# Kernel optimization log

Measured on AMD Instinct MI355X. Metric: run time of the kernel, lower is better.

The kernel has to match this reference:

```python
import jax, jax.numpy as jnp
import numpy as np

B, T, F = 2048, 2048, 12   # n_locations, seq_len, input features
E, P, H = 4, 4, 4          # embedding_dim, pre_hidden, n_hidden
D1, D3, OUT = 4, 6, 1      # hidden dense sizes, output_dim


def setup_inputs() -> dict:
    key = jax.random.key(0)
    ks = jax.random.split(key, 14)
    s = lambda k, shape, fan_in: jax.random.normal(k, shape, jnp.float32) / np.sqrt(fan_in)
    return {
        "x": jax.random.normal(ks[0], (B, T, F), jnp.float32),
        "embed": s(ks[1], (B, E), 1.0),            # Embed table, rows = arange(n_locations)
        "W1": s(ks[2], (F + E, D1), F + E), "b1": jnp.zeros((D1,), jnp.float32),
        "W2": s(ks[3], (D1, P), D1),        "b2": jnp.zeros((P,), jnp.float32),
        "Wi": s(ks[4], (P, H), P),          "bi": jnp.zeros((H,), jnp.float32),
        "Wh": s(ks[5], (H, H), H),          # SimpleCell h2h has no bias in flax
        "W3": s(ks[6], (H, D3), H),         "b3": jnp.zeros((D3,), jnp.float32),
        "W4": s(ks[7], (D3, OUT), D3),      "b4": jnp.zeros((OUT,), jnp.float32),
    }


def reference(x, embed, W1, b1, W2, b2, Wi, bi, Wh, W3, b3, W4, b4):
    # loc = Embed(arange(n_locations)) -> the full table; broadcast over time.
    Tn = x.shape[1]
    loc = jnp.broadcast_to(embed[:, None, :], (embed.shape[0], Tn, embed.shape[1]))
    h = jnp.concatenate([x, loc], axis=-1)            # [B, T, F+E]
    h = jax.nn.relu(h @ W1 + b1)                      # Dense(4) + relu (dropout: no-op, deterministic)
    h = h @ W2 + b2                                   # Dense(pre_hidden)
    # SimpleCell: h_t = tanh(Dense_i(x_t) + Dense_h(h_{t-1})); precompute input proj.
    xi = h @ Wi + bi                                  # [B, T, H]
    h0 = jnp.zeros((x.shape[0], Wh.shape[0]), x.dtype)

    def step(carry, xt):
        new_h = jnp.tanh(xt + carry @ Wh)
        return new_h, new_h

    _, ys = jax.lax.scan(step, h0, jnp.swapaxes(xi, 0, 1))  # scan over time: [T, B, H]
    y = jnp.swapaxes(ys, 0, 1)                        # [B, T, H]
    y = jax.nn.relu(y @ W3 + b3)                      # Dense(6) + relu
    return y @ W4 + b4                                # Dense(output_dim)
```

## Files before the change

### kernel.cpp

```cpp
#include <hip/hip_runtime.h>
#include <hip/hip_fp16.h>


using u32 = unsigned int;
using u16 = unsigned short;

#define B_N 2048
#define T_N 2048

typedef __fp16 f16x2 __attribute__((ext_vector_type(2)));

__device__ __forceinline__ float bfh(u16 v){ return __uint_as_float(((u32)v) << 16); }
__device__ __forceinline__ float lo16(u32 u){ return __uint_as_float(u << 16); }
__device__ __forceinline__ float hi16(u32 u){ return __uint_as_float(u & 0xFFFF0000u); }
__device__ __forceinline__ u16 f2bf(float f){
  u32 u = __float_as_uint(f);
  return (u16)((u + 0x7FFFu + ((u >> 16) & 1u)) >> 16);
}
__device__ __forceinline__ float h2f(u16 h){ return __half2float(__ushort_as_half(h)); }
__device__ __forceinline__ u32 pk2(float a, float b){
  union { f16x2 h; u32 u; } cv;
  cv.h = __builtin_amdgcn_cvt_pkrtz(a, b);
  return cv.u;
}

__global__ void k_setup(const void* __restrict__ xraw,
                        const void* __restrict__ embed, const void* __restrict__ W1,
                        const void* __restrict__ b1, const void* __restrict__ W2,
                        const void* __restrict__ b2, const void* __restrict__ Wi,
                        const void* __restrict__ bi, const void* __restrict__ Wh,
                        const void* __restrict__ W3, const void* __restrict__ b3,
                        const void* __restrict__ W4, const void* __restrict__ b4,
                        float* __restrict__ cbuf)
{
  const float S = 2.8853900817779268f;
  const int tid = threadIdx.x;
  __shared__ float sflag;

  if (tid < 64) {
    const u16* xu = (const u16*)xraw;
    u32 e = (xu[2*tid] >> 7) & 0xFF;
    unsigned long long m = __ballot(e >= 110 && e <= 140);
    if (tid == 0) {
      float f = (__popcll(m) < 32) ? 1.0f : 0.0f;
      sflag = f;
      cbuf[126] = f;
    }
  }
  __syncthreads();
  const bool f32 = sflag > 0.5f;
  auto ld = [&](const void* p, int i) -> float {
    return f32 ? ((const float*)p)[i] : bfh(((const u16*)p)[i]);
  };

  if (tid < 48) {
    cbuf[tid] = ld(W1, tid);
  } else if (tid < 64) {
    int i = tid - 48, r = i >> 2, c = i & 3;
    float s = 0.f;
    for (int p = 0; p < 4; ++p) s += ld(W2, r*4+p) * ld(Wi, p*4+c);
    cbuf[48 + i] = S * s;
  } else if (tid < 68) {
    int c = tid - 64;
    float s = ld(bi, c);
    for (int p = 0; p < 4; ++p) s += ld(b2, p) * ld(Wi, p*4+c);
    float sw = 0.f;
    for (int k = 0; k < 4; ++k) sw += ld(Wh, k*4+c);
    cbuf[64 + c] = S * s + S * sw;
  } else if (tid < 84) {
    int i = tid - 68;
    cbuf[68 + i] = -2.f * S * ld(Wh, i);
  } else if (tid < 108) {
    cbuf[tid] = ld(W3, tid - 84);
  } else if (tid < 114) {
    cbuf[tid] = ld(b3, tid - 108);
  } else if (tid < 120) {
    cbuf[tid] = ld(W4, tid - 114);
  } else if (tid == 120) {
    cbuf[120] = ld(b4, 0);
  }
  for (int b = tid; b < B_N; b += blockDim.x) {
    for (int c = 0; c < 4; ++c) {
      float s = ld(b1, c);
      for (int e = 0; e < 4; ++e) s += ld(embed, b*4+e) * ld(W1, (12+e)*4+c);
      cbuf[128 + b*4 + c] = s;
    }
  }
}

__global__ __launch_bounds__(256) void k_xi(const void* __restrict__ xraw,
                                            const float* __restrict__ cbuf,
                                            float* __restrict__ xi2)
{
  __shared__ u32 sx[12320];
  const int tid = threadIdx.x;
  const int b0 = (blockIdx.x >> 4) << 3;
  const int t0 = (blockIdx.x & 15) << 7;
  const bool f32 = cbuf[126] > 0.5f;

  const int RS  = f32 ? 1540 : 772;
  const int CPT = f32 ? 12 : 6;
  const int K   = f32 ? 12 : 6;

  {
    const int r = tid >> 5, c = tid & 31;
    const size_t rowbase_u32 = ((size_t)(b0 + r) * T_N + t0) * (size_t)CPT;
    const uint4* gsrc = (const uint4*)((const u32*)xraw + rowbase_u32);
    uint4* ldst = (uint4*)(sx + r * RS);
    for (int k = 0; k < K; ++k)
      ldst[c + 32*k] = gsrc[c + 32*k];
  }
  __syncthreads();

  float W1f[48];
#pragma unroll
  for (int i = 0; i < 48; ++i) W1f[i] = cbuf[i];
  float Wc[16];
#pragma unroll
  for (int i = 0; i < 16; ++i) Wc[i] = cbuf[48+i];
  float bc[4];
#pragma unroll
  for (int i = 0; i < 4; ++i) bc[i] = cbuf[64+i];

  const int r = tid & 7, t4l = tid >> 3;
  const int b = b0 + r;
  const int T4 = (t0 >> 2) + t4l;
  float p1[4];
#pragma unroll
  for (int i = 0; i < 4; ++i) p1[i] = cbuf[128 + b*4 + i];

  float acc[4][4];
#pragma unroll
  for (int ti = 0; ti < 4; ++ti) {
    const u32* sp = sx + r * RS + (t4l*4 + ti) * CPT;
    float xf[12];
    if (f32) {
#pragma unroll
      for (int f = 0; f < 12; ++f) xf[f] = __uint_as_float(sp[f]);
    } else {
#pragma unroll
      for (int w = 0; w < 6; ++w) {
        u32 u = sp[w];
        xf[2*w]   = lo16(u);
        xf[2*w+1] = hi16(u);
      }
    }
    float h1[4];
#pragma unroll
    for (int c = 0; c < 4; ++c) {
      float s = p1[c];
#pragma unroll
      for (int f = 0; f < 12; ++f) s = fmaf(xf[f], W1f[f*4+c], s);
      h1[c] = fmaxf(s, 0.f);
    }
#pragma unroll
    for (int c = 0; c < 4; ++c) {
      float s = bc[c];
#pragma unroll
      for (int k = 0; k < 4; ++k) s = fmaf(h1[k], Wc[k*4+c], s);
      acc[c][ti] = s;
    }
  }
  float4* dst = (float4*)xi2 + ((size_t)T4 * B_N + b) * 4;
#pragma unroll
  for (int jj = 0; jj < 4; ++jj)
    dst[jj] = make_float4(acc[jj][0], acc[jj][1], acc[jj][2], acc[jj][3]);
}

template<int CTRL>
__device__ __forceinline__ float dppf(float v) {
  return __int_as_float(__builtin_amdgcn_mov_dpp(__float_as_int(v), CTRL, 0xF, 0xF, true));
}

__global__ __launch_bounds__(64) void k_scan(const float* __restrict__ cbuf,
                                             const float* __restrict__ xi2,
                                             u32* __restrict__ hbuf)
{
  const int g = blockIdx.x * 64 + threadIdx.x;
  const int b = g >> 2, j = g & 3;
  const float u0 = cbuf[68 + (j<<2) + j];
  const float u1 = cbuf[68 + ((j^1)<<2) + j];
  const float u2 = cbuf[68 + ((j^2)<<2) + j];
  const float u3 = cbuf[68 + ((j^3)<<2) + j];

  const float4* xp = (const float4*)xi2 + (size_t)b*4 + j;
  uint2* hp = (uint2*)hbuf + (size_t)b * (T_N/4) * 4 + j;

  constexpr int D = 8;
  float4 buf[D];
#pragma unroll
  for (int i = 0; i < D; ++i) buf[i] = xp[(size_t)i * (B_N*4)];

  float r = 0.5f;
  for (int tb = 0; tb < T_N/4; tb += D) {
#pragma unroll
    for (int q = 0; q < D; ++q) {
      float4 xiv = buf[q];
      int pf = tb + q + D; pf = pf < (T_N/4 - 1) ? pf : (T_N/4 - 1);
      buf[q] = xp[(size_t)pf * (B_N*4)];
      float bases[4] = {xiv.x, xiv.y, xiv.z, xiv.w};
      float hv[4];
#pragma unroll
      for (int ti = 0; ti < 4; ++ti) {
        float rs  = r;
        float rx1 = dppf<0xB1>(rs);
        float rx2 = dppf<0x4E>(rs);
        float rx3 = dppf<0x1B>(rs);
        float pa = fmaf(u0, rs,  bases[ti]);
        float pb = fmaf(u1, rx1, pa);
        float pc = u2 * rx2;
        float pd = fmaf(u3, rx3, pc);
        float z  = pb + pd;
        float e  = __builtin_amdgcn_exp2f(z);
        r = __builtin_amdgcn_rcpf(e + 1.0f);
        hv[ti] = fmaf(-2.0f, r, 1.0f);
      }
      hp[(size_t)(tb + q) * 4] = make_uint2(pk2(hv[0], hv[1]), pk2(hv[2], hv[3]));
    }
  }
}

__global__ __launch_bounds__(256) void k_out(const u32* __restrict__ hbuf,
                                             const float* __restrict__ cbuf,
                                             void* __restrict__ outp)
{
  const int g = blockIdx.x * 256 + threadIdx.x;
  const int b = g >> 9;
  const int t4 = g & 511;
  const bool f32 = cbuf[126] > 0.5f;

  float W3f[24], b3f[6], W4f[6];
#pragma unroll
  for (int i = 0; i < 24; ++i) W3f[i] = cbuf[84+i];
#pragma unroll
  for (int i = 0; i < 6; ++i)  b3f[i] = cbuf[108+i];
#pragma unroll
  for (int i = 0; i < 6; ++i)  W4f[i] = cbuf[114+i];
  const float b4f = cbuf[120];

  const uint4* hp = (const uint4*)hbuf + (size_t)(b * 512 + t4) * 2;
  uint4 q0 = hp[0], q1 = hp[1];
  u32 wj[4][2] = {{q0.x,q0.y},{q0.z,q0.w},{q1.x,q1.y},{q1.z,q1.w}};

  float res[4];
#pragma unroll
  for (int s = 0; s < 4; ++s) {
    float h0 = h2f((u16)(wj[0][s>>1] >> ((s&1)*16)));
    float h1 = h2f((u16)(wj[1][s>>1] >> ((s&1)*16)));
    float h2 = h2f((u16)(wj[2][s>>1] >> ((s&1)*16)));
    float h3 = h2f((u16)(wj[3][s>>1] >> ((s&1)*16)));
    float a = b4f;
#pragma unroll
    for (int m = 0; m < 6; ++m) {
      float y = b3f[m];
      y = fmaf(h0, W3f[0*6+m], y);
      y = fmaf(h1, W3f[1*6+m], y);
      y = fmaf(h2, W3f[2*6+m], y);
      y = fmaf(h3, W3f[3*6+m], y);
      y = fmaxf(y, 0.f);
      a = fmaf(y, W4f[m], a);
    }
    res[s] = a;
  }
  if (f32) {
    *((float4*)outp + ((size_t)b * 512 + t4)) = make_float4(res[0], res[1], res[2], res[3]);
  } else {
    uint2 pk;
    pk.x = (u32)f2bf(res[0]) | ((u32)f2bf(res[1]) << 16);
    pk.y = (u32)f2bf(res[2]) | ((u32)f2bf(res[3]) << 16);
    *((uint2*)outp + ((size_t)b * 512 + t4)) = pk;
  }
}

extern "C" void kernel_launch(void* const* d_in, const int* in_sizes, int n_in,
                              void* d_out, int out_size, void* d_ws, size_t ws_size,
                              hipStream_t stream)
{
  float* cbuf = (float*)d_ws;
  float* xi2  = (float*)((char*)d_ws + 65536);
  u32*   hbuf = (u32*)((char*)d_ws + 65536 + (size_t)B_N*T_N*16);

  k_setup<<<1, 256, 0, stream>>>(d_in[0], d_in[1], d_in[2], d_in[3], d_in[4],
                                 d_in[5], d_in[6], d_in[7], d_in[8], d_in[9],
                                 d_in[10], d_in[11], d_in[12], cbuf);
  k_xi  <<<4096, 256, 0, stream>>>(d_in[0], cbuf, xi2);
  k_scan<<<128, 64, 0, stream>>>(cbuf, xi2, (u32*)hbuf);
  k_out <<<4096, 256, 0, stream>>>(hbuf, cbuf, d_out);
}
```

Baseline: 408.9 us.

## Store xi intermediate as fp16 and fold setup kernel into consumers

Drops the separate single-block setup kernel. Each consumer kernel now probes the input dtype and builds its own constants in shared memory or registers. The xi intermediate written by k_xi and read by the latency-bound scan is packed to fp16, which halves its footprint and the bandwidth the scan's strided loads need. This removes one launch and its serialization, at the cost of redundant per-block constant computation and lower precision in the recurrence inputs.

```diff
diff --git a/kernel.cpp b/kernel.cpp
--- a/kernel.cpp
+++ b/kernel.cpp
@@ -17,86 +17,73 @@
   u32 u = __float_as_uint(f);
   return (u16)((u + 0x7FFFu + ((u >> 16) & 1u)) >> 16);
 }
-__device__ __forceinline__ float h2f(u16 h){ return __half2float(__ushort_as_half(h)); }
 __device__ __forceinline__ u32 pk2(float a, float b){
   union { f16x2 h; u32 u; } cv;
   cv.h = __builtin_amdgcn_cvt_pkrtz(a, b);
   return cv.u;
 }
-
-__global__ void k_setup(const void* __restrict__ xraw,
-                        const void* __restrict__ embed, const void* __restrict__ W1,
-                        const void* __restrict__ b1, const void* __restrict__ W2,
-                        const void* __restrict__ b2, const void* __restrict__ Wi,
-                        const void* __restrict__ bi, const void* __restrict__ Wh,
-                        const void* __restrict__ W3, const void* __restrict__ b3,
-                        const void* __restrict__ W4, const void* __restrict__ b4,
-                        float* __restrict__ cbuf)
-{
-  const float S = 2.8853900817779268f;
-  const int tid = threadIdx.x;
-  __shared__ float sflag;
-
-  if (tid < 64) {
-    const u16* xu = (const u16*)xraw;
-    u32 e = (xu[2*tid] >> 7) & 0xFF;
-    unsigned long long m = __ballot(e >= 110 && e <= 140);
-    if (tid == 0) {
-      float f = (__popcll(m) < 32) ? 1.0f : 0.0f;
-      sflag = f;
-      cbuf[126] = f;
-    }
-  }
-  __syncthreads();
-  const bool f32 = sflag > 0.5f;
-  auto ld = [&](const void* p, int i) -> float {
-    return f32 ? ((const float*)p)[i] : bfh(((const u16*)p)[i]);
-  };
-
-  if (tid < 48) {
-    cbuf[tid] = ld(W1, tid);
-  } else if (tid < 64) {
-    int i = tid - 48, r = i >> 2, c = i & 3;
-    float s = 0.f;
-    for (int p = 0; p < 4; ++p) s += ld(W2, r*4+p) * ld(Wi, p*4+c);
-    cbuf[48 + i] = S * s;
-  } else if (tid < 68) {
-    int c = tid - 64;
-    float s = ld(bi, c);
-    for (int p = 0; p < 4; ++p) s += ld(b2, p) * ld(Wi, p*4+c);
-    float sw = 0.f;
-    for (int k = 0; k < 4; ++k) sw += ld(Wh, k*4+c);
-    cbuf[64 + c] = S * s + S * sw;
-  } else if (tid < 84) {
-    int i = tid - 68;
-    cbuf[68 + i] = -2.f * S * ld(Wh, i);
-  } else if (tid < 108) {
-    cbuf[tid] = ld(W3, tid - 84);
-  } else if (tid < 114) {
-    cbuf[tid] = ld(b3, tid - 108);
-  } else if (tid < 120) {
-    cbuf[tid] = ld(W4, tid - 114);
-  } else if (tid == 120) {
-    cbuf[120] = ld(b4, 0);
-  }
-  for (int b = tid; b < B_N; b += blockDim.x) {
-    for (int c = 0; c < 4; ++c) {
-      float s = ld(b1, c);
-      for (int e = 0; e < 4; ++e) s += ld(embed, b*4+e) * ld(W1, (12+e)*4+c);
-      cbuf[128 + b*4 + c] = s;
-    }
-  }
+__device__ __forceinline__ float xlo(u32 w){ return __half2float(__ushort_as_half((u16)(w & 0xFFFFu))); }
+__device__ __forceinline__ float xhi(u32 w){ return __half2float(__ushort_as_half((u16)(w >> 16))); }
+
+#define S_PRE 2.8853900817779268f
+#define S_NEG (-5.7707801635558537f)
+
+__device__ __forceinline__ bool probe_f32(const void* xraw, int lane){
+  const u16* xu = (const u16*)xraw;
+  u32 e = (xu[2*lane] >> 7) & 0xFF;
+  unsigned long long m = __ballot(e >= 110 && e <= 140);
+  return __popcll(m) < 32;
+}
+__device__ __forceinline__ float ldsel(const void* p, int i, bool f32){
+  return f32 ? ((const float*)p)[i] : bfh(((const u16*)p)[i]);
 }
 
 __global__ __launch_bounds__(256) void k_xi(const void* __restrict__ xraw,
-                                            const float* __restrict__ cbuf,
-                                            float* __restrict__ xi2)
+                                            const void* __restrict__ embed,
+                                            const void* __restrict__ W1,
+                                            const void* __restrict__ b1,
+                                            const void* __restrict__ W2,
+                                            const void* __restrict__ b2,
+                                            const void* __restrict__ Wi,
+                                            const void* __restrict__ bi,
+                                            const void* __restrict__ Wh,
+                                            u32* __restrict__ xi2)
 {
   __shared__ u32 sx[12320];
+  __shared__ float sc[104];
   const int tid = threadIdx.x;
   const int b0 = (blockIdx.x >> 4) << 3;
   const int t0 = (blockIdx.x & 15) << 7;
-  const bool f32 = cbuf[126] > 0.5f;
+
+  if (tid < 64) {
+    const bool f32 = probe_f32(xraw, tid);
+    if (tid == 0) sc[100] = f32 ? 1.0f : 0.0f;
+    if (tid < 48) sc[tid] = ldsel(W1, tid, f32);
+    else {
+      int i = tid - 48, r = i >> 2, c = i & 3;
+      float s = 0.f;
+      for (int p = 0; p < 4; ++p) s += ldsel(W2, r*4+p, f32) * ldsel(Wi, p*4+c, f32);
+      sc[48 + i] = S_PRE * s;
+    }
+    if (tid < 4) {
+      int c = tid;
+      float s = ldsel(bi, c, f32);
+      for (int p = 0; p < 4; ++p) s += ldsel(b2, p, f32) * ldsel(Wi, p*4+c, f32);
+      float sw = 0.f;
+      for (int k = 0; k < 4; ++k) sw += ldsel(Wh, k*4+c, f32);
+      sc[64 + c] = S_PRE * (s + sw);
+    }
+    if (tid < 32) {
+      int r = tid >> 2, c = tid & 3;
+      int b = b0 + r;
+      float s = ldsel(b1, c, f32);
+      for (int e = 0; e < 4; ++e)
+        s += ldsel(embed, b*4+e, f32) * ldsel(W1, (12+e)*4+c, f32);
+      sc[68 + tid] = s;
+    }
+  }
+  __syncthreads();
+  const bool f32 = sc[100] > 0.5f;
 
   const int RS  = f32 ? 1540 : 772;
   const int CPT = f32 ? 12 : 6;
@@ -114,20 +101,20 @@
 
   float W1f[48];
 #pragma unroll
-  for (int i = 0; i < 48; ++i) W1f[i] = cbuf[i];
+  for (int i = 0; i < 48; ++i) W1f[i] = sc[i];
   float Wc[16];
 #pragma unroll
-  for (int i = 0; i < 16; ++i) Wc[i] = cbuf[48+i];
+  for (int i = 0; i < 16; ++i) Wc[i] = sc[48+i];
   float bc[4];
 #pragma unroll
-  for (int i = 0; i < 4; ++i) bc[i] = cbuf[64+i];
+  for (int i = 0; i < 4; ++i) bc[i] = sc[64+i];
 
   const int r = tid & 7, t4l = tid >> 3;
   const int b = b0 + r;
   const int T4 = (t0 >> 2) + t4l;
   float p1[4];
 #pragma unroll
-  for (int i = 0; i < 4; ++i) p1[i] = cbuf[128 + b*4 + i];
+  for (int i = 0; i < 4; ++i) p1[i] = sc[68 + r*4 + i];
 
   float acc[4][4];
 #pragma unroll
@@ -161,10 +148,15 @@
       acc[c][ti] = s;
     }
   }
-  float4* dst = (float4*)xi2 + ((size_t)T4 * B_N + b) * 4;
-#pragma unroll
-  for (int jj = 0; jj < 4; ++jj)
-    dst[jj] = make_float4(acc[jj][0], acc[jj][1], acc[jj][2], acc[jj][3]);
+  u32 w[8];
+#pragma unroll
+  for (int j = 0; j < 4; ++j) {
+    w[j*2]   = pk2(acc[j][0], acc[j][1]);
+    w[j*2+1] = pk2(acc[j][2], acc[j][3]);
+  }
+  u32* dst = xi2 + ((size_t)T4 * B_N + b) * 8;
+  *(uint4*)(dst)     = make_uint4(w[0], w[1], w[2], w[3]);
+  *(uint4*)(dst + 4) = make_uint4(w[4], w[5], w[6], w[7]);
 }
 
 template<int CTRL>
@@ -172,22 +164,26 @@
   return __int_as_float(__builtin_amdgcn_mov_dpp(__float_as_int(v), CTRL, 0xF, 0xF, true));
 }
 
-__global__ __launch_bounds__(64) void k_scan(const float* __restrict__ cbuf,
-                                             const float* __restrict__ xi2,
+__global__ __launch_bounds__(64) void k_scan(const void* __restrict__ xraw,
+                                             const void* __restrict__ Wh,
+                                             const u32* __restrict__ xi2,
                                              u32* __restrict__ hbuf)
 {
-  const int g = blockIdx.x * 64 + threadIdx.x;
+  const int tid = threadIdx.x;
+  const bool f32 = probe_f32(xraw, tid);
+
+  const int g = blockIdx.x * 64 + tid;
   const int b = g >> 2, j = g & 3;
-  const float u0 = cbuf[68 + (j<<2) + j];
-  const float u1 = cbuf[68 + ((j^1)<<2) + j];
-  const float u2 = cbuf[68 + ((j^2)<<2) + j];
-  const float u3 = cbuf[68 + ((j^3)<<2) + j];
-
-  const float4* xp = (const float4*)xi2 + (size_t)b*4 + j;
+  const float u0 = S_NEG * ldsel(Wh, (j<<2) + j, f32);
+  const float u1 = S_NEG * ldsel(Wh, ((j^1)<<2) + j, f32);
+  const float u2 = S_NEG * ldsel(Wh, ((j^2)<<2) + j, f32);
+  const float u3 = S_NEG * ldsel(Wh, ((j^3)<<2) + j, f32);
+
+  const uint2* xp = (const uint2*)xi2 + (size_t)b*4 + j;
   uint2* hp = (uint2*)hbuf + (size_t)b * (T_N/4) * 4 + j;
 
   constexpr int D = 8;
-  float4 buf[D];
+  uint2 buf[D];
 #pragma unroll
   for (int i = 0; i < D; ++i) buf[i] = xp[(size_t)i * (B_N*4)];
 
@@ -195,10 +191,10 @@
   for (int tb = 0; tb < T_N/4; tb += D) {
 #pragma unroll
     for (int q = 0; q < D; ++q) {
-      float4 xiv = buf[q];
+      uint2 xiv = buf[q];
       int pf = tb + q + D; pf = pf < (T_N/4 - 1) ? pf : (T_N/4 - 1);
       buf[q] = xp[(size_t)pf * (B_N*4)];
-      float bases[4] = {xiv.x, xiv.y, xiv.z, xiv.w};
+      float bases[4] = {xlo(xiv.x), xhi(xiv.x), xlo(xiv.y), xhi(xiv.y)};
       float hv[4];
 #pragma unroll
       for (int ti = 0; ti < 4; ++ti) {
@@ -220,23 +216,39 @@
   }
 }
 
-__global__ __launch_bounds__(256) void k_out(const u32* __restrict__ hbuf,
-                                             const float* __restrict__ cbuf,
+__global__ __launch_bounds__(256) void k_out(const void* __restrict__ xraw,
+                                             const void* __restrict__ W3,
+                                             const void* __restrict__ b3,
+                                             const void* __restrict__ W4,
+                                             const void* __restrict__ b4,
+                                             const u32* __restrict__ hbuf,
                                              void* __restrict__ outp)
 {
-  const int g = blockIdx.x * 256 + threadIdx.x;
+  __shared__ float sc[40];
+  const int tid = threadIdx.x;
+  if (tid < 64) {
+    const bool f32 = probe_f32(xraw, tid);
+    if (tid == 0) sc[37] = f32 ? 1.0f : 0.0f;
+    if (tid < 24)                sc[tid]      = ldsel(W3, tid, f32);
+    else if (tid < 30)           sc[tid]      = ldsel(b3, tid - 24, f32);
+    else if (tid < 36)           sc[tid]      = ldsel(W4, tid - 30, f32);
+    else if (tid == 36)          sc[36]       = ldsel(b4, 0, f32);
+  }
+  __syncthreads();
+  const bool f32 = sc[37] > 0.5f;
+
+  float W3f[24], b3f[6], W4f[6];
+#pragma unroll
+  for (int i = 0; i < 24; ++i) W3f[i] = sc[i];
+#pragma unroll
+  for (int i = 0; i < 6; ++i)  b3f[i] = sc[24+i];
+#pragma unroll
+  for (int i = 0; i < 6; ++i)  W4f[i] = sc[30+i];
+  const float b4f = sc[36];
+
+  const int g = blockIdx.x * 256 + tid;
   const int b = g >> 9;
   const int t4 = g & 511;
-  const bool f32 = cbuf[126] > 0.5f;
-
-  float W3f[24], b3f[6], W4f[6];
-#pragma unroll
-  for (int i = 0; i < 24; ++i) W3f[i] = cbuf[84+i];
-#pragma unroll
-  for (int i = 0; i < 6; ++i)  b3f[i] = cbuf[108+i];
-#pragma unroll
-  for (int i = 0; i < 6; ++i)  W4f[i] = cbuf[114+i];
-  const float b4f = cbuf[120];
 
   const uint4* hp = (const uint4*)hbuf + (size_t)(b * 512 + t4) * 2;
   uint4 q0 = hp[0], q1 = hp[1];
@@ -245,10 +257,10 @@
   float res[4];
 #pragma unroll
   for (int s = 0; s < 4; ++s) {
-    float h0 = h2f((u16)(wj[0][s>>1] >> ((s&1)*16)));
-    float h1 = h2f((u16)(wj[1][s>>1] >> ((s&1)*16)));
-    float h2 = h2f((u16)(wj[2][s>>1] >> ((s&1)*16)));
-    float h3 = h2f((u16)(wj[3][s>>1] >> ((s&1)*16)));
+    float h0 = (s&1) ? xhi(wj[0][s>>1]) : xlo(wj[0][s>>1]);
+    float h1 = (s&1) ? xhi(wj[1][s>>1]) : xlo(wj[1][s>>1]);
+    float h2 = (s&1) ? xhi(wj[2][s>>1]) : xlo(wj[2][s>>1]);
+    float h3 = (s&1) ? xhi(wj[3][s>>1]) : xlo(wj[3][s>>1]);
     float a = b4f;
 #pragma unroll
     for (int m = 0; m < 6; ++m) {
@@ -276,14 +288,12 @@
                               void* d_out, int out_size, void* d_ws, size_t ws_size,
                               hipStream_t stream)
 {
-  float* cbuf = (float*)d_ws;
-  float* xi2  = (float*)((char*)d_ws + 65536);
-  u32*   hbuf = (u32*)((char*)d_ws + 65536 + (size_t)B_N*T_N*16);
-
-  k_setup<<<1, 256, 0, stream>>>(d_in[0], d_in[1], d_in[2], d_in[3], d_in[4],
-                                 d_in[5], d_in[6], d_in[7], d_in[8], d_in[9],
-                                 d_in[10], d_in[11], d_in[12], cbuf);
-  k_xi  <<<4096, 256, 0, stream>>>(d_in[0], cbuf, xi2);
-  k_scan<<<128, 64, 0, stream>>>(cbuf, xi2, (u32*)hbuf);
-  k_out <<<4096, 256, 0, stream>>>(hbuf, cbuf, d_out);
-}
+  u32* xi2  = (u32*)d_ws;
+  u32* hbuf = (u32*)((char*)d_ws + (size_t)B_N*T_N*4*2);
+
+  k_xi  <<<4096, 256, 0, stream>>>(d_in[0], d_in[1], d_in[2], d_in[3], d_in[4],
+                                   d_in[5], d_in[6], d_in[7], d_in[8], xi2);
+  k_scan<<<128, 64, 0, stream>>>(d_in[0], d_in[8], xi2, hbuf);
+  k_out <<<4096, 256, 0, stream>>>(d_in[0], d_in[9], d_in[10], d_in[11], d_in[12],
+                                   hbuf, d_out);
+}
```

Result: faster. 388.9 us (-4.9%).
